# Optimization experiments

Hardware: AMD Instinct MI355X
Metric: run time of the kernel (lower is better)

Reference implementation:

```python
import jax, jax.numpy as jnp
import numpy as np

N_NODES = 50000
N_EDGES = 800000
NFEAT, NHID, NCLASS = 128, 256, 64


def setup_inputs() -> dict:
    key = jax.random.key(0)
    ks = jax.random.split(key, 8)
    x = jax.random.normal(ks[0], (N_NODES, NFEAT), dtype=jnp.float32)
    edge_index = jax.random.randint(ks[1], (2, N_EDGES), 0, N_NODES, dtype=jnp.int64)
    s1 = 1.0 / np.sqrt(NFEAT)
    s2 = 1.0 / np.sqrt(NHID)
    W1_neigh = jax.random.normal(ks[2], (NFEAT, NHID), dtype=jnp.float32) * s1
    W1_root = jax.random.normal(ks[3], (NFEAT, NHID), dtype=jnp.float32) * s1
    b1 = jnp.zeros((NHID,), dtype=jnp.float32)
    W2_neigh = jax.random.normal(ks[4], (NHID, NCLASS), dtype=jnp.float32) * s2
    W2_root = jax.random.normal(ks[5], (NHID, NCLASS), dtype=jnp.float32) * s2
    b2 = jnp.zeros((NCLASS,), dtype=jnp.float32)
    return {"x": x, "edge_index": edge_index, "W1_neigh": W1_neigh,
            "W1_root": W1_root, "b1": b1, "W2_neigh": W2_neigh,
            "W2_root": W2_root, "b2": b2}


def _sage_conv(h, src, dst, n_nodes, W_neigh, W_root, b):
    # mean aggregation of source features into destination nodes
    msg = h[src]                                                   # [E, d]
    summed = jax.ops.segment_sum(msg, dst, num_segments=n_nodes)   # [N, d]
    cnt = jax.ops.segment_sum(jnp.ones((src.shape[0],), h.dtype), dst,
                              num_segments=n_nodes)                # [N]
    mean = summed / jnp.maximum(cnt, 1.0)[:, None]
    return mean @ W_neigh + h @ W_root + b


def reference(x, edge_index, W1_neigh, W1_root, b1, W2_neigh, W2_root, b2):
    src, dst = edge_index[0], edge_index[1]
    n = x.shape[0]
    h = jax.nn.relu(_sage_conv(x, src, dst, n, W1_neigh, W1_root, b1))
    # dropout is identity in eval mode
    out = _sage_conv(h, src, dst, n, W2_neigh, W2_root, b2)
    return out
```

## Files before the change

kernel.cpp:

```cpp
#include <hip/hip_runtime.h>

#define N_NODES 50000
#define N_EDGES 800000
#define NFEAT   128
#define NHID    256
#define NCLASS  64

#define ELLCAP  64

#define NBUCK   56
#define BWIDTH  896
#define BCAP    16384
#define BIN_CH  4096
#define BIN_B   ((N_EDGES + BIN_CH - 1) / BIN_CH)
#define NFINE   ((N_NODES + 127) / 128)
#define NFINE2  ((N_NODES + 63) / 64)
#define FPB     7

#define CVTX_B  ((N_NODES * 32 + 255) / 256)
#define CVTW_B  (((65536 + 32768) + 255) / 256)

typedef unsigned short u16;
typedef unsigned int   u32;
typedef __attribute__((ext_vector_type(8))) short s16x8;
typedef __attribute__((ext_vector_type(4))) float f32x4;

__device__ inline u16 f2bf(float f) {
    u32 u = __float_as_uint(f);
    u32 r = (u + 0x7FFFu + ((u >> 16) & 1u)) >> 16;
    return (u16)r;
}
__device__ inline float bflo(u32 v) { return __uint_as_float(v << 16); }
__device__ inline float bfhi(u32 v) { return __uint_as_float(v & 0xFFFF0000u); }

#define GLOAD_LDS16(g, l)                                                        \
    __builtin_amdgcn_global_load_lds(                                            \
        (const __attribute__((address_space(1))) u32*)(const void*)(g),          \
        (__attribute__((address_space(3))) u32*)(void*)(l), 16, 0, 0)

__global__ __launch_bounds__(256) void prep_kernel(const float* __restrict__ x,
                                                   const int* __restrict__ ei,
                                                   const float* __restrict__ W1r,
                                                   const float* __restrict__ W1n,
                                                   const float* __restrict__ W2n,
                                                   const float* __restrict__ W2r,
                                                   u16* __restrict__ xa,
                                                   u32* __restrict__ gcnt,
                                                   u32* __restrict__ bbuf,
                                                   u16* __restrict__ W1t,
                                                   u16* __restrict__ W2t) {
    int b = blockIdx.x;
    if (b < BIN_B) {
        __shared__ u32 hist[NBUCK];
        __shared__ u32 base[NBUCK];
        int tid = threadIdx.x;
        if (tid < NBUCK) hist[tid] = 0;
        __syncthreads();
        u32 ek[16]; u32 rk[16]; int bk[16];
        int i0 = b * BIN_CH;
        #pragma unroll
        for (int k = 0; k < 16; ++k) {
            int i = i0 + k * 256 + tid;
            bk[k] = -1;
            if (i < N_EDGES) {
                u32 s = (u32)ei[i];
                u32 d = (u32)ei[N_EDGES + i];
                int bu = (int)(d / BWIDTH);
                ek[k] = (d << 16) | s;
                bk[k] = bu;
                rk[k] = atomicAdd(&hist[bu], 1u);
            }
        }
        __syncthreads();
        if (tid < NBUCK) base[tid] = atomicAdd(&gcnt[tid], hist[tid]);
        __syncthreads();
        #pragma unroll
        for (int k = 0; k < 16; ++k) {
            if (bk[k] >= 0) {
                u32 pos = base[bk[k]] + rk[k];
                if (pos < BCAP) bbuf[((u32)bk[k] << 14) + pos] = ek[k];
            }
        }
    } else if (b < BIN_B + CVTX_B) {
        int idx = (b - BIN_B) * 256 + threadIdx.x;
        if (idx >= N_NODES * 32) return;
        int r  = idx >> 5;
        int c4 = (idx & 31) * 4;
        float4 v = *reinterpret_cast<const float4*>(x + (size_t)r * NFEAT + c4);
        uint2 o;
        o.x = (u32)f2bf(v.x) | ((u32)f2bf(v.y) << 16);
        o.y = (u32)f2bf(v.z) | ((u32)f2bf(v.w) << 16);
        *reinterpret_cast<uint2*>(xa + (size_t)r * 256 + c4) = o;
    } else {
        int id = (b - BIN_B - CVTX_B) * 256 + threadIdx.x;
        if (id < 65536) {
            int k = id & 255, n = id >> 8;
            float v = (k < NFEAT) ? W1r[(size_t)k * NHID + n]
                                  : W1n[(size_t)(k - NFEAT) * NHID + n];
            W1t[(size_t)n * 256 + k] = f2bf(v);
        } else if (id < 65536 + 32768) {
            int j = id - 65536;
            int k = j & 255, n = j >> 8;
            float v = (n < NCLASS) ? W2n[(size_t)k * NCLASS + n]
                                   : W2r[(size_t)k * NCLASS + (n - NCLASS)];
            W2t[(size_t)n * 256 + k] = f2bf(v);
        }
    }
}

__global__ __launch_bounds__(512) void ell_build_kernel(const u32* __restrict__ bbuf,
                                                        const u32* __restrict__ gcnt,
                                                        int* __restrict__ cnt,
                                                        u16* __restrict__ ell) {
    __shared__ u32 hist[128];
    int tid = threadIdx.x;
    int f   = blockIdx.x;
    int cb  = f / FPB;
    int n0  = f * 128;
    if (tid < 128) hist[tid] = 0;
    __syncthreads();
    int m = (int)gcnt[cb]; if (m > BCAP) m = BCAP;
    const u32* bk = bbuf + ((u32)cb << 14);
    int i = tid;
    for (; i + 1536 < m; i += 2048) {
        u32 e0 = bk[i], e1 = bk[i + 512], e2 = bk[i + 1024], e3 = bk[i + 1536];
        u32 d0 = (e0 >> 16) - (u32)n0, d1 = (e1 >> 16) - (u32)n0;
        u32 d2 = (e2 >> 16) - (u32)n0, d3 = (e3 >> 16) - (u32)n0;
        if (d0 < 128u) { u32 p = atomicAdd(&hist[d0], 1u); if (p < ELLCAP) ell[(size_t)(n0 + (int)d0) * ELLCAP + p] = (u16)e0; }
        if (d1 < 128u) { u32 p = atomicAdd(&hist[d1], 1u); if (p < ELLCAP) ell[(size_t)(n0 + (int)d1) * ELLCAP + p] = (u16)e1; }
        if (d2 < 128u) { u32 p = atomicAdd(&hist[d2], 1u); if (p < ELLCAP) ell[(size_t)(n0 + (int)d2) * ELLCAP + p] = (u16)e2; }
        if (d3 < 128u) { u32 p = atomicAdd(&hist[d3], 1u); if (p < ELLCAP) ell[(size_t)(n0 + (int)d3) * ELLCAP + p] = (u16)e3; }
    }
    for (; i < m; i += 512) {
        u32 e = bk[i];
        u32 d = (e >> 16) - (u32)n0;
        if (d < 128u) { u32 p = atomicAdd(&hist[d], 1u); if (p < ELLCAP) ell[(size_t)(n0 + (int)d) * ELLCAP + p] = (u16)e; }
    }
    __syncthreads();
    if (tid < 128) cnt[n0 + tid] = (int)hist[tid];
}

#define ACC8(v)                                                      \
    do { a[0] += bflo((v).x); a[1] += bfhi((v).x);                   \
         a[2] += bflo((v).y); a[3] += bfhi((v).y);                   \
         a[4] += bflo((v).z); a[5] += bfhi((v).z);                   \
         a[6] += bflo((v).w); a[7] += bfhi((v).w); } while (0)

__global__ __launch_bounds__(256) void gather1_kernel(const int* __restrict__ cnt,
                                                      const u16* __restrict__ ell,
                                                      u16* __restrict__ xa) {
    int gtid = blockIdx.x * 256 + threadIdx.x;
    int node = gtid >> 6;
    if (node >= N_NODES) return;
    int lane = threadIdx.x & 63;
    int g = lane >> 4, lr = lane & 15;
    const u32* xrow = reinterpret_cast<const u32*>(xa);
    const u16* idx = ell + (size_t)node * ELLCAP;
    int deg = cnt[node];
    if (deg > ELLCAP) deg = ELLCAP;
    float a[8] = {};
    int j = 0;
    for (; j + 16 <= deg; j += 16) {
        int s0 = idx[j + g], s1 = idx[j + 4 + g], s2 = idx[j + 8 + g], s3 = idx[j + 12 + g];
        uint4 v0 = *reinterpret_cast<const uint4*>(xrow + (size_t)s0 * 128 + lr * 4);
        uint4 v1 = *reinterpret_cast<const uint4*>(xrow + (size_t)s1 * 128 + lr * 4);
        uint4 v2 = *reinterpret_cast<const uint4*>(xrow + (size_t)s2 * 128 + lr * 4);
        uint4 v3 = *reinterpret_cast<const uint4*>(xrow + (size_t)s3 * 128 + lr * 4);
        ACC8(v0); ACC8(v1); ACC8(v2); ACC8(v3);
    }
    for (; j + 4 <= deg; j += 4) {
        int s0 = idx[j + g];
        uint4 v0 = *reinterpret_cast<const uint4*>(xrow + (size_t)s0 * 128 + lr * 4);
        ACC8(v0);
    }
    if (g < deg - j) {
        int s0 = idx[j + g];
        uint4 v0 = *reinterpret_cast<const uint4*>(xrow + (size_t)s0 * 128 + lr * 4);
        ACC8(v0);
    }
    #pragma unroll
    for (int k = 0; k < 8; ++k) {
        a[k] += __shfl_xor(a[k], 16);
        a[k] += __shfl_xor(a[k], 32);
    }
    if (g == 0) {
        float invd = 1.0f / fmaxf((float)deg, 1.0f);
        uint4 pk;
        pk.x = (u32)f2bf(a[0] * invd) | ((u32)f2bf(a[1] * invd) << 16);
        pk.y = (u32)f2bf(a[2] * invd) | ((u32)f2bf(a[3] * invd) << 16);
        pk.z = (u32)f2bf(a[4] * invd) | ((u32)f2bf(a[5] * invd) << 16);
        pk.w = (u32)f2bf(a[6] * invd) | ((u32)f2bf(a[7] * invd) << 16);
        *reinterpret_cast<uint4*>(reinterpret_cast<u32*>(xa) + (size_t)node * 128 + 64 + lr * 4) = pk;
    }
}

__global__ __launch_bounds__(256) void gather2_kernel(const int* __restrict__ cnt,
                                                      const u16* __restrict__ ell,
                                                      const u16* __restrict__ t,
                                                      float* __restrict__ out) {
    int gtid = blockIdx.x * 256 + threadIdx.x;
    int node = gtid >> 6;
    if (node >= N_NODES) return;
    int lane = threadIdx.x & 63;
    int g = lane >> 3, lr = lane & 7;
    const u32* trow = reinterpret_cast<const u32*>(t);
    const u16* idx = ell + (size_t)node * ELLCAP;
    int deg = cnt[node];
    if (deg > ELLCAP) deg = ELLCAP;
    float a[8] = {};
    int j = 0;
    for (; j + 16 <= deg; j += 16) {
        int s0 = idx[j + g], s1 = idx[j + 8 + g];
        uint4 v0 = *reinterpret_cast<const uint4*>(trow + (size_t)s0 * 32 + lr * 4);
        uint4 v1 = *reinterpret_cast<const uint4*>(trow + (size_t)s1 * 32 + lr * 4);
        ACC8(v0); ACC8(v1);
    }
    for (; j + 8 <= deg; j += 8) {
        int s0 = idx[j + g];
        uint4 v0 = *reinterpret_cast<const uint4*>(trow + (size_t)s0 * 32 + lr * 4);
        ACC8(v0);
    }
    if (g < deg - j) {
        int s0 = idx[j + g];
        uint4 v0 = *reinterpret_cast<const uint4*>(trow + (size_t)s0 * 32 + lr * 4);
        ACC8(v0);
    }
    #pragma unroll
    for (int k = 0; k < 8; ++k) {
        a[k] += __shfl_xor(a[k], 8);
        a[k] += __shfl_xor(a[k], 16);
        a[k] += __shfl_xor(a[k], 32);
    }
    if (g == 0) {
        float invd = 1.0f / fmaxf((float)deg, 1.0f);
        float* o = out + (size_t)node * NCLASS + lr * 8;
        float4 o0 = *reinterpret_cast<float4*>(o);
        float4 o1 = *reinterpret_cast<float4*>(o + 4);
        o0.x += a[0] * invd; o0.y += a[1] * invd; o0.z += a[2] * invd; o0.w += a[3] * invd;
        o1.x += a[4] * invd; o1.y += a[5] * invd; o1.z += a[6] * invd; o1.w += a[7] * invd;
        *reinterpret_cast<float4*>(o) = o0;
        *reinterpret_cast<float4*>(o + 4) = o1;
    }
}

__global__ __launch_bounds__(256, 3) void gemm12_fused(const u16* __restrict__ xa,
                                                       const u16* __restrict__ W1t,
                                                       const float* __restrict__ b1,
                                                       const u16* __restrict__ W2t,
                                                       const float* __restrict__ b2,
                                                       u16* __restrict__ t,
                                                       float* __restrict__ out) {
    __shared__ u16 hs[64 * 256];
    const int tid = threadIdx.x;
    const int r0 = blockIdx.x * 64;
    const int wid = tid >> 6, ln = tid & 63;
    const int lr = ln & 15;
    const int lq = ln >> 4;

    const int wn1 = wid * 64;
    {
        f32x4 acc[4][4] = {};
        #pragma unroll
        for (int ks = 0; ks < 8; ++ks) {
            const int k0 = ks * 32;
            s16x8 af[4], bf[4];
            #pragma unroll
            for (int i = 0; i < 4; ++i)
                af[i] = *reinterpret_cast<const s16x8*>(
                    xa + (size_t)(r0 + i * 16 + lr) * 256 + k0 + lq * 8);
            #pragma unroll
            for (int j = 0; j < 4; ++j)
                bf[j] = *reinterpret_cast<const s16x8*>(
                    W1t + (size_t)(wn1 + j * 16 + lr) * 256 + k0 + lq * 8);
            #pragma unroll
            for (int i = 0; i < 4; ++i)
                #pragma unroll
                for (int j = 0; j < 4; ++j)
                    acc[i][j] = __builtin_amdgcn_mfma_f32_16x16x32_bf16(
                        af[i], bf[j], acc[i][j], 0, 0, 0);
        }
        #pragma unroll
        for (int j = 0; j < 4; ++j) {
            int col = wn1 + j * 16 + lr;
            float bias = b1[col];
            #pragma unroll
            for (int i = 0; i < 4; ++i)
                #pragma unroll
                for (int r = 0; r < 4; ++r) {
                    int row = i * 16 + lq * 4 + r;
                    hs[row * 256 + (col ^ ((row & 7) << 3))] =
                        f2bf(fmaxf(acc[i][j][r] + bias, 0.0f));
                }
        }
    }
    __syncthreads();

    const int wn2 = wid * 32;
    f32x4 acc[4][2] = {};
    #pragma unroll
    for (int ks = 0; ks < 8; ++ks) {
        const int k0 = ks * 32;
        s16x8 af[4], bf[2];
        #pragma unroll
        for (int i = 0; i < 4; ++i) {
            int row = i * 16 + lr;
            af[i] = *reinterpret_cast<const s16x8*>(
                hs + row * 256 + ((k0 + lq * 8) ^ ((row & 7) << 3)));
        }
        #pragma unroll
        for (int j = 0; j < 2; ++j)
            bf[j] = *reinterpret_cast<const s16x8*>(
                W2t + (size_t)(wn2 + j * 16 + lr) * 256 + k0 + lq * 8);
        #pragma unroll
        for (int i = 0; i < 4; ++i)
            #pragma unroll
            for (int j = 0; j < 2; ++j)
                acc[i][j] = __builtin_amdgcn_mfma_f32_16x16x32_bf16(
                    af[i], bf[j], acc[i][j], 0, 0, 0);
    }

    #pragma unroll
    for (int i = 0; i < 4; ++i) {
        #pragma unroll
        for (int j = 0; j < 2; ++j) {
            int col = wn2 + j * 16 + lr;
            #pragma unroll
            for (int r = 0; r < 4; ++r) {
                int row = r0 + i * 16 + lq * 4 + r;
                if (row >= N_NODES) continue;
                if (col < NCLASS) {
                    t[(size_t)row * NCLASS + col] = f2bf(acc[i][j][r]);
                } else {
                    int c = col - NCLASS;
                    out[(size_t)row * NCLASS + c] = acc[i][j][r] + b2[c];
                }
            }
        }
    }
}

extern "C" void kernel_launch(void* const* d_in, const int* in_sizes, int n_in,
                              void* d_out, int out_size, void* d_ws, size_t ws_size,
                              hipStream_t stream) {
    const float* x    = (const float*)d_in[0];
    const int*   ei   = (const int*)d_in[1];
    const float* W1n  = (const float*)d_in[2];
    const float* W1r  = (const float*)d_in[3];
    const float* b1   = (const float*)d_in[4];
    const float* W2n  = (const float*)d_in[5];
    const float* W2r  = (const float*)d_in[6];
    const float* b2   = (const float*)d_in[7];
    float* out = (float*)d_out;

    u32* gcnt = (u32*)d_ws;
    u32* bbuf = gcnt + 64;
    int* cnt  = (int*)(bbuf + ((size_t)NBUCK << 14));
    u16* ell  = (u16*)(cnt + 50048);
    u16* xa   = ell + (size_t)N_NODES * ELLCAP;
    u16* t    = xa + (size_t)50048 * 256;
    u16* W1t  = t  + (size_t)N_NODES * 64;
    u16* W2t  = W1t + 65536;

    hipMemsetAsync(gcnt, 0, 64 * sizeof(u32), stream);

    prep_kernel<<<BIN_B + CVTX_B + CVTW_B, 256, 0, stream>>>(
        x, ei, W1r, W1n, W2n, W2r, xa, gcnt, bbuf, W1t, W2t);
    ell_build_kernel<<<NFINE, 512, 0, stream>>>(bbuf, gcnt, cnt, ell);

    gather1_kernel<<<(N_NODES * 64 + 255) / 256, 256, 0, stream>>>(cnt, ell, xa);

    gemm12_fused<<<NFINE2, 256, 0, stream>>>(xa, W1t, b1, W2t, b2, t, out);

    gather2_kernel<<<(N_NODES * 64 + 255) / 256, 256, 0, stream>>>(cnt, ell, t, out);
}
```

Before: 201.5 us.

## Split fused two-layer GEMM into separate kernels with hidden activations in global memory

```diff
diff --git a/kernel.cpp b/kernel.cpp
--- a/kernel.cpp
+++ b/kernel.cpp
@@ -14,7 +14,6 @@
 #define BIN_CH  4096
 #define BIN_B   ((N_EDGES + BIN_CH - 1) / BIN_CH)
 #define NFINE   ((N_NODES + 127) / 128)
-#define NFINE2  ((N_NODES + 63) / 64)
 #define FPB     7
 
 #define CVTX_B  ((N_NODES * 32 + 255) / 256)
@@ -32,11 +31,6 @@
 }
 __device__ inline float bflo(u32 v) { return __uint_as_float(v << 16); }
 __device__ inline float bfhi(u32 v) { return __uint_as_float(v & 0xFFFF0000u); }
-
-#define GLOAD_LDS16(g, l)                                                        \
-    __builtin_amdgcn_global_load_lds(                                            \
-        (const __attribute__((address_space(1))) u32*)(const void*)(g),          \
-        (__attribute__((address_space(3))) u32*)(void*)(l), 16, 0, 0)
 
 __global__ __launch_bounds__(256) void prep_kernel(const float* __restrict__ x,
                                                    const int* __restrict__ ei,
@@ -243,90 +237,90 @@
     }
 }
 
-__global__ __launch_bounds__(256, 3) void gemm12_fused(const u16* __restrict__ xa,
-                                                       const u16* __restrict__ W1t,
-                                                       const float* __restrict__ b1,
-                                                       const u16* __restrict__ W2t,
-                                                       const float* __restrict__ b2,
-                                                       u16* __restrict__ t,
-                                                       float* __restrict__ out) {
-    __shared__ u16 hs[64 * 256];
+__global__ __launch_bounds__(256, 5) void gemm1_nolds(const u16* __restrict__ xa,
+                                                      const u16* __restrict__ W1t,
+                                                      const float* __restrict__ b1,
+                                                      u16* __restrict__ h) {
     const int tid = threadIdx.x;
-    const int r0 = blockIdx.x * 64;
     const int wid = tid >> 6, ln = tid & 63;
-    const int lr = ln & 15;
-    const int lq = ln >> 4;
-
-    const int wn1 = wid * 64;
-    {
-        f32x4 acc[4][4] = {};
-        #pragma unroll
-        for (int ks = 0; ks < 8; ++ks) {
-            const int k0 = ks * 32;
-            s16x8 af[4], bf[4];
-            #pragma unroll
-            for (int i = 0; i < 4; ++i)
-                af[i] = *reinterpret_cast<const s16x8*>(
-                    xa + (size_t)(r0 + i * 16 + lr) * 256 + k0 + lq * 8);
+    const int lr = ln & 15, lq = ln >> 4;
+    const int rb = blockIdx.x * 32;
+    const int wn = wid * 64;
+    const u16* ar = xa + (size_t)rb * 256;
+    const u16* br = W1t + (size_t)wn * 256;
+
+    f32x4 acc[2][4] = {};
+    #pragma unroll
+    for (int ks = 0; ks < 8; ++ks) {
+        const int k0 = ks * 32;
+        s16x8 af[2], bf[4];
+        #pragma unroll
+        for (int i = 0; i < 2; ++i)
+            af[i] = *reinterpret_cast<const s16x8*>(ar + (size_t)(i * 16 + lr) * 256 + k0 + lq * 8);
+        #pragma unroll
+        for (int j = 0; j < 4; ++j)
+            bf[j] = *reinterpret_cast<const s16x8*>(br + (size_t)(j * 16 + lr) * 256 + k0 + lq * 8);
+        #pragma unroll
+        for (int i = 0; i < 2; ++i)
             #pragma unroll
             for (int j = 0; j < 4; ++j)
-                bf[j] = *reinterpret_cast<const s16x8*>(
-                    W1t + (size_t)(wn1 + j * 16 + lr) * 256 + k0 + lq * 8);
+                acc[i][j] = __builtin_amdgcn_mfma_f32_16x16x32_bf16(af[i], bf[j], acc[i][j], 0, 0, 0);
+    }
+
+    #pragma unroll
+    for (int j = 0; j < 4; ++j) {
+        int col = wn + j * 16 + lr;
+        float bias = b1[col];
+        #pragma unroll
+        for (int i = 0; i < 2; ++i)
             #pragma unroll
-            for (int i = 0; i < 4; ++i)
-                #pragma unroll
-                for (int j = 0; j < 4; ++j)
-                    acc[i][j] = __builtin_amdgcn_mfma_f32_16x16x32_bf16(
-                        af[i], bf[j], acc[i][j], 0, 0, 0);
-        }
-        #pragma unroll
-        for (int j = 0; j < 4; ++j) {
-            int col = wn1 + j * 16 + lr;
-            float bias = b1[col];
-            #pragma unroll
-            for (int i = 0; i < 4; ++i)
-                #pragma unroll
-                for (int r = 0; r < 4; ++r) {
-                    int row = i * 16 + lq * 4 + r;
-                    hs[row * 256 + (col ^ ((row & 7) << 3))] =
-                        f2bf(fmaxf(acc[i][j][r] + bias, 0.0f));
-                }
-        }
-    }
-    __syncthreads();
-
-    const int wn2 = wid * 32;
-    f32x4 acc[4][2] = {};
+            for (int r = 0; r < 4; ++r) {
+                int row = rb + i * 16 + lq * 4 + r;
+                if (row < N_NODES)
+                    h[(size_t)row * 256 + col] = f2bf(fmaxf(acc[i][j][r] + bias, 0.0f));
+            }
+    }
+}
+
+__global__ __launch_bounds__(256, 5) void gemm2_nolds(const u16* __restrict__ h,
+                                                      const u16* __restrict__ W2t,
+                                                      const float* __restrict__ b2,
+                                                      u16* __restrict__ t,
+                                                      float* __restrict__ out) {
+    const int tid = threadIdx.x;
+    const int wid = tid >> 6, ln = tid & 63;
+    const int lr = ln & 15, lq = ln >> 4;
+    const int rb = blockIdx.x * 64 + (wid >> 1) * 32;
+    const int wn = (wid & 1) * 64;
+    const u16* ar = h + (size_t)rb * 256;
+    const u16* br = W2t + (size_t)wn * 256;
+
+    f32x4 acc[2][4] = {};
     #pragma unroll
     for (int ks = 0; ks < 8; ++ks) {
         const int k0 = ks * 32;
-        s16x8 af[4], bf[2];
-        #pragma unroll
-        for (int i = 0; i < 4; ++i) {
-            int row = i * 16 + lr;
-            af[i] = *reinterpret_cast<const s16x8*>(
-                hs + row * 256 + ((k0 + lq * 8) ^ ((row & 7) << 3)));
-        }
-        #pragma unroll
-        for (int j = 0; j < 2; ++j)
-            bf[j] = *reinterpret_cast<const s16x8*>(
-                W2t + (size_t)(wn2 + j * 16 + lr) * 256 + k0 + lq * 8);
-        #pragma unroll
-        for (int i = 0; i < 4; ++i)
+        s16x8 af[2], bf[4];
+        #pragma unroll
+        for (int i = 0; i < 2; ++i)
+            af[i] = *reinterpret_cast<const s16x8*>(ar + (size_t)(i * 16 + lr) * 256 + k0 + lq * 8);
+        #pragma unroll
+        for (int j = 0; j < 4; ++j)
+            bf[j] = *reinterpret_cast<const s16x8*>(br + (size_t)(j * 16 + lr) * 256 + k0 + lq * 8);
+        #pragma unroll
+        for (int i = 0; i < 2; ++i)
             #pragma unroll
-            for (int j = 0; j < 2; ++j)
-                acc[i][j] = __builtin_amdgcn_mfma_f32_16x16x32_bf16(
-                    af[i], bf[j], acc[i][j], 0, 0, 0);
-    }
-
-    #pragma unroll
-    for (int i = 0; i < 4; ++i) {
-        #pragma unroll
-        for (int j = 0; j < 2; ++j) {
-            int col = wn2 + j * 16 + lr;
+            for (int j = 0; j < 4; ++j)
+                acc[i][j] = __builtin_amdgcn_mfma_f32_16x16x32_bf16(af[i], bf[j], acc[i][j], 0, 0, 0);
+    }
+
+    #pragma unroll
+    for (int i = 0; i < 2; ++i) {
+        #pragma unroll
+        for (int j = 0; j < 4; ++j) {
+            int col = wn + j * 16 + lr;
             #pragma unroll
             for (int r = 0; r < 4; ++r) {
-                int row = r0 + i * 16 + lq * 4 + r;
+                int row = rb + i * 16 + lq * 4 + r;
                 if (row >= N_NODES) continue;
                 if (col < NCLASS) {
                     t[(size_t)row * NCLASS + col] = f2bf(acc[i][j][r]);
@@ -357,7 +351,8 @@
     int* cnt  = (int*)(bbuf + ((size_t)NBUCK << 14));
     u16* ell  = (u16*)(cnt + 50048);
     u16* xa   = ell + (size_t)N_NODES * ELLCAP;
-    u16* t    = xa + (size_t)50048 * 256;
+    u16* h    = xa + (size_t)50048 * 256;
+    u16* t    = h  + (size_t)50048 * 256;
     u16* W1t  = t  + (size_t)N_NODES * 64;
     u16* W2t  = W1t + 65536;
 
@@ -368,8 +363,8 @@
     ell_build_kernel<<<NFINE, 512, 0, stream>>>(bbuf, gcnt, cnt, ell);
 
     gather1_kernel<<<(N_NODES * 64 + 255) / 256, 256, 0, stream>>>(cnt, ell, xa);
-
-    gemm12_fused<<<NFINE2, 256, 0, stream>>>(xa, W1t, b1, W2t, b2, t, out);
-
+    gemm1_nolds<<<(N_NODES + 31) / 32, 256, 0, stream>>>(xa, W1t, b1, h);
+
+    gemm2_nolds<<<(N_NODES + 63) / 64, 256, 0, stream>>>(h, W2t, b2, t, out);
     gather2_kernel<<<(N_NODES * 64 + 255) / 256, 256, 0, stream>>>(cnt, ell, t, out);
 }
```

Result: slower. 235.6 us (+17.0%).
